# Kernel tuning notes

Measured on AMD Instinct MI355X. Metric: run time of the kernel, lower is better.

The kernel has to match this reference:

```python
import jax, jax.numpy as jnp
import numpy as np

DIM = 256
KEY_DIM = 16
NUM_HEADS = 8
ATTN_RATIO = 4
NH_KD = KEY_DIM * NUM_HEADS   # 128
D = ATTN_RATIO * KEY_DIM      # 64
DH = D * NUM_HEADS            # 512
POS_LEN = 16
SCALE = KEY_DIM ** -0.5


def _cbn(x, w, s, b):
    # 1x1 conv (no bias) + folded BatchNorm affine. w: [out,in], x: [B,in,H,W]
    y = jnp.einsum('oi,bihw->bohw', w, x)
    return y * s[None, :, None, None] + b[None, :, None, None]


def _interp_pos(pos, n):
    # F.interpolate(mode='linear', align_corners=False) from length POS_LEN to n.
    L = pos.shape[-1]
    coords = (jnp.arange(n, dtype=pos.dtype) + 0.5) * (L / n) - 0.5
    coords = jnp.clip(coords, 0.0, L - 1)
    lo = jnp.floor(coords).astype(jnp.int32)
    hi = jnp.minimum(lo + 1, L - 1)
    t = coords - lo.astype(pos.dtype)
    return pos[..., lo] * (1 - t) + pos[..., hi] * t  # [1,C,n]


def _axial_attn(q_emb, k_emb, v_emb, pos_q, pos_k, n):
    # q_emb/k_emb: [B,NH_KD,n], v_emb: [B,DH,n]
    B = q_emb.shape[0]
    q = (q_emb + _interp_pos(pos_q, n)).reshape(B, NUM_HEADS, KEY_DIM, n)
    k = (k_emb + _interp_pos(pos_k, n)).reshape(B, NUM_HEADS, KEY_DIM, n)
    v = v_emb.reshape(B, NUM_HEADS, D, n)
    attn = jnp.einsum('bhcn,bhcm->bhnm', q, k) * SCALE
    attn = jax.nn.softmax(attn, axis=-1)
    xx = jnp.einsum('bhnm,bhdm->bhnd', attn, v)      # [B,NH,n,D]
    return xx.transpose(0, 1, 3, 2).reshape(B, DH, n)  # [B,DH,n]


def _forward(x, wq, sq, bq, wk, sk, bk, wv, sv, bv,
             pos_rowq, pos_rowk, pos_colq, pos_colk,
             w_row, s_row, b_row, w_col, s_col, b_col,
             w_proj, s_proj, b_proj, w_sc, s_sc, b_sc,
             w_dw, s_dw, b_dw, w_pw, s_pw, b_pw):
    B, C, H, W = x.shape
    q = _cbn(x, wq, sq, bq)   # [B,NH_KD,H,W]
    k = _cbn(x, wk, sk, bk)
    v = _cbn(x, wv, sv, bv)   # [B,DH,H,W]

    # row branch (mean over W)
    xx_row = _axial_attn(q.mean(-1), k.mean(-1), v.mean(-1), pos_rowq, pos_rowk, H)
    xx_row = _cbn(jax.nn.relu(xx_row[..., None]), w_row, s_row, b_row)      # [B,DH,H,1]
    # column branch (mean over H)
    xx_col = _axial_attn(q.mean(-2), k.mean(-2), v.mean(-2), pos_colq, pos_colk, W)
    xx_col = _cbn(jax.nn.relu(xx_col[:, :, None, :]), w_col, s_col, b_col)  # [B,DH,1,W]

    attn_out = v + (xx_row + xx_col)
    attn_out = _cbn(jax.nn.relu(attn_out), w_proj, s_proj, b_proj)          # [B,DIM,H,W]

    # gate branch: 1x1 -> dw3x3 -> relu -> 1x1 -> h_sigmoid
    gate = _cbn(x, w_sc, s_sc, b_sc)
    gate = jax.lax.conv_general_dilated(
        gate, w_dw, (1, 1), 'SAME',
        dimension_numbers=('NCHW', 'OIHW', 'NCHW'), feature_group_count=DIM)
    gate = gate * s_dw[None, :, None, None] + b_dw[None, :, None, None]
    gate = jax.nn.relu(gate)
    gate = _cbn(gate, w_pw, s_pw, b_pw)
    gate = jnp.clip(gate + 3.0, 0.0, 6.0) / 6.0  # h_sigmoid
    return gate * attn_out


def setup_inputs() -> dict:
    key = jax.random.key(0)
    ks = jax.random.split(key, 32)
    B, H, W = 16, 64, 64
    nrm = lambda k, sh, sc=0.05: jax.random.normal(k, sh, dtype=jnp.float32) * sc
    inp = {
        'x': nrm(ks[0], (B, DIM, H, W), 1.0),
        'wq': nrm(ks[1], (NH_KD, DIM)), 'sq': 1.0 + nrm(ks[2], (NH_KD,)), 'bq': nrm(ks[3], (NH_KD,)),
        'wk': nrm(ks[4], (NH_KD, DIM)), 'sk': 1.0 + nrm(ks[5], (NH_KD,)), 'bk': nrm(ks[6], (NH_KD,)),
        'wv': nrm(ks[7], (DH, DIM)), 'sv': 1.0 + nrm(ks[8], (DH,)), 'bv': nrm(ks[9], (DH,)),
        'pos_rowq': nrm(ks[10], (1, NH_KD, POS_LEN), 1.0), 'pos_rowk': nrm(ks[11], (1, NH_KD, POS_LEN), 1.0),
        'pos_colq': nrm(ks[12], (1, NH_KD, POS_LEN), 1.0), 'pos_colk': nrm(ks[13], (1, NH_KD, POS_LEN), 1.0),
        'w_row': nrm(ks[14], (DH, DH)), 's_row': 1.0 + nrm(ks[15], (DH,)), 'b_row': nrm(ks[16], (DH,)),
        'w_col': nrm(ks[17], (DH, DH)), 's_col': 1.0 + nrm(ks[18], (DH,)), 'b_col': nrm(ks[19], (DH,)),
        'w_proj': nrm(ks[20], (DIM, DH)), 's_proj': 1.0 + nrm(ks[21], (DIM,)), 'b_proj': nrm(ks[22], (DIM,)),
        'w_sc': nrm(ks[23], (DIM, DIM)), 's_sc': 1.0 + nrm(ks[24], (DIM,)), 'b_sc': nrm(ks[25], (DIM,)),
        'w_dw': nrm(ks[26], (DIM, 1, 3, 3)), 's_dw': 1.0 + nrm(ks[27], (DIM,)), 'b_dw': nrm(ks[28], (DIM,)),
        'w_pw': nrm(ks[29], (DIM, DIM)), 's_pw': 1.0 + nrm(ks[30], (DIM,)), 'b_pw': nrm(ks[31], (DIM,)),
    }
    return inp


def reference(x, wq, sq, bq, wk, sk, bk, wv, sv, bv,
              pos_rowq, pos_rowk, pos_colq, pos_colk,
              w_row, s_row, b_row, w_col, s_col, b_col,
              w_proj, s_proj, b_proj, w_sc, s_sc, b_sc,
              w_dw, s_dw, b_dw, w_pw, s_pw, b_pw):
    return _forward(x, wq, sq, bq, wk, sk, bk, wv, sv, bv,
                    pos_rowq, pos_rowk, pos_colq, pos_colk,
                    w_row, s_row, b_row, w_col, s_col, b_col,
                    w_proj, s_proj, b_proj, w_sc, s_sc, b_sc,
                    w_dw, s_dw, b_dw, w_pw, s_pw, b_pw)
```

## Files before the change

### kernel.cpp

```cpp
#include <hip/hip_runtime.h>
#include <math.h>

typedef unsigned short u16;
typedef unsigned int u32;
typedef short short8 __attribute__((ext_vector_type(8)));
typedef float f32x4 __attribute__((ext_vector_type(4)));

#define Bn 16
#define Cc 256
#define Pp 4096
#define DHc 512
#define PTOT 65536
#define SCALE 0.25f

__device__ __forceinline__ float bf2f(u16 u) {
    return __uint_as_float(((u32)u) << 16);
}
__device__ __forceinline__ u16 f2bf(float f) {
    u32 u = __float_as_uint(f);
    u32 lsb = (u >> 16) & 1u;
    u += 0x7fffu + lsb;
    return (u16)(u >> 16);
}

__device__ __forceinline__ void gload16(const u16* g, u16* l) {
    __builtin_amdgcn_global_load_lds(
        (const __attribute__((address_space(1))) void*)(uintptr_t)g,
        (__attribute__((address_space(3))) void*)(u32)(uintptr_t)l,
        16, 0, 0);
}

__global__ __launch_bounds__(256) void mean_kernel(
    const float* __restrict__ x, u16* __restrict__ xmb) {
    __shared__ float plane[64][65];
    int bc = blockIdx.x;
    int b = bc >> 8, c = bc & 255;
    const float* xp = x + (size_t)bc * Pp;
    int tid = threadIdx.x;
#pragma unroll
    for (int k = 0; k < 16; ++k) {
        int idx = tid + k * 256;
        plane[idx >> 6][idx & 63] = xp[idx];
    }
    __syncthreads();
    if (tid < 64) {
        float s = 0.f;
#pragma unroll
        for (int w = 0; w < 64; ++w) s += plane[tid][w];
        xmb[((size_t)b * 64 + tid) * 256 + c] = f2bf(s * (1.f / 64.f));
    } else if (tid < 128) {
        int w = tid - 64;
        float s = 0.f;
#pragma unroll
        for (int h = 0; h < 64; ++h) s += plane[h][w];
        xmb[((size_t)1024 + b * 64 + w) * 256 + c] = f2bf(s * (1.f / 64.f));
    }
}

__global__ __launch_bounds__(256) void xpose_kernel(
    const float* __restrict__ x, u16* __restrict__ xbf) {
    __shared__ float tile[64][65];
    int pb = blockIdx.x;
    int cb = blockIdx.y;
    int b = blockIdx.z;
    int t = threadIdx.x;
    int p_l = t & 63, c_q = t >> 6;
    const float* xp = x + ((size_t)b * Cc + cb * 64) * Pp + pb * 64;
#pragma unroll
    for (int rr = 0; rr < 16; ++rr) {
        int c_l = rr * 4 + c_q;
        tile[p_l][c_l] = xp[(size_t)c_l * Pp + p_l];
    }
    __syncthreads();
    int c_l2 = t & 63, p_q = t >> 6;
    u16* dst = xbf + ((size_t)b * Pp + pb * 64) * Cc + cb * 64;
#pragma unroll
    for (int rr = 0; rr < 16; ++rr) {
        int p_l2 = rr * 4 + p_q;
        dst[(size_t)p_l2 * Cc + c_l2] = f2bf(tile[p_l2][c_l2]);
    }
}

__global__ __launch_bounds__(256) void wconv_kernel(
    const float* __restrict__ wq, const float* __restrict__ wk, const float* __restrict__ wv,
    const float* __restrict__ wsc, const float* __restrict__ wproj, const float* __restrict__ wpw,
    const float* __restrict__ wrow, const float* __restrict__ wcol,
    const float* __restrict__ wdw,
    u16* __restrict__ wqkvb, u16* __restrict__ wscb,
    u16* __restrict__ wprojb, u16* __restrict__ wpwb,
    u16* __restrict__ wrb, u16* __restrict__ wcb, float* __restrict__ wdwT) {
    int t = blockIdx.x * 256 + threadIdx.x;
    if (t < 2304) wdwT[(t % 9) * 256 + (t / 9)] = wdw[t];
    if (t < 32768) wqkvb[t] = f2bf(wq[t]);
    else if (t < 65536) wqkvb[t] = f2bf(wk[t - 32768]);
    else if (t < 196608) wqkvb[t] = f2bf(wv[t - 65536]);
    else if (t < 262144) wscb[t - 196608] = f2bf(wsc[t - 196608]);
    else if (t < 393216) wprojb[t - 262144] = f2bf(wproj[t - 262144]);
    else if (t < 458752) wpwb[t - 393216] = f2bf(wpw[t - 393216]);
    else if (t < 720896) wrb[t - 458752] = f2bf(wrow[t - 458752]);
    else wcb[t - 720896] = f2bf(wcol[t - 720896]);
}

__device__ __forceinline__ void gemm_mainloop(
    const u16* __restrict__ W, const u16* __restrict__ X, int K,
    int o0, size_t prow0, u16* ldsA, u16* ldsB, f32x4 (&acc)[4][4]) {
    int t = threadIdx.x;
    int w = t >> 6, lane = t & 63;
    int sr = (w << 5) + (lane >> 2);
    int ks = (lane & 3) * 8;
    const u16* gA = W + (size_t)(o0 + sr) * K + ks;
    const u16* gB = X + (prow0 + sr) * K + ks;
    u16* lA = ldsA + sr * 32 + ks;
    u16* lB = ldsB + sr * 32 + ks;
    int wo = (w >> 1) * 64, wp = (w & 1) * 64;
    const u16* fA = ldsA + (wo + (lane & 15)) * 32 + ((lane >> 4) * 8);
    const u16* fB = ldsB + (wp + (lane & 15)) * 32 + ((lane >> 4) * 8);

    for (int k0 = 0; k0 < K; k0 += 32) {
        if (k0) __syncthreads();
        gload16(gA + k0, lA);
        gload16(gA + k0 + (size_t)16 * K, lA + 16 * 32);
        gload16(gB + k0, lB);
        gload16(gB + k0 + (size_t)16 * K, lB + 16 * 32);
        __syncthreads();
        short8 a[4], b[4];
#pragma unroll
        for (int i = 0; i < 4; ++i) a[i] = *(const short8*)(fA + i * 16 * 32);
#pragma unroll
        for (int j = 0; j < 4; ++j) b[j] = *(const short8*)(fB + j * 16 * 32);
#pragma unroll
        for (int i = 0; i < 4; ++i)
#pragma unroll
            for (int j = 0; j < 4; ++j)
                acc[i][j] = __builtin_amdgcn_mfma_f32_16x16x32_bf16(a[i], b[j], acc[i][j], 0, 0, 0);
    }
}

__global__ __launch_bounds__(256) void gemm_qkv(
    const u16* __restrict__ Wb, const u16* __restrict__ X,
    const float* __restrict__ sq, const float* __restrict__ bq,
    const float* __restrict__ sk, const float* __restrict__ bk,
    const float* __restrict__ sv, const float* __restrict__ bv,
    const float* __restrict__ posrq, const float* __restrict__ posrk,
    const float* __restrict__ poscq, const float* __restrict__ posck,
    float* __restrict__ qrow, float* __restrict__ krow, float* __restrict__ vrow,
    float* __restrict__ qcol, float* __restrict__ kcol, float* __restrict__ vcol) {
    __shared__ u16 ldsA[128 * 32];
    __shared__ u16 ldsB[128 * 32];
    f32x4 acc[4][4];
#pragma unroll
    for (int i = 0; i < 4; ++i)
#pragma unroll
        for (int j = 0; j < 4; ++j) acc[i][j] = (f32x4){0.f, 0.f, 0.f, 0.f};
    int o0 = blockIdx.x * 128;
    size_t prow0 = (size_t)blockIdx.y * 128;
    gemm_mainloop(Wb, X, 256, o0, prow0, ldsA, ldsB, acc);

    int lane = threadIdx.x & 63, w = threadIdx.x >> 6;
    int wo = (w >> 1) * 64, wp = (w & 1) * 64;
    int quad = lane >> 4, cn = lane & 15;
#pragma unroll
    for (int j = 0; j < 4; ++j) {
        int p = (int)prow0 + wp + j * 16 + cn;
        int branch = p >> 10, loc = p & 1023;
        int b = loc >> 6, n = loc & 63;
        float coords = 0.25f * (float)n - 0.375f;
        coords = fminf(fmaxf(coords, 0.f), 15.f);
        int lo = (int)floorf(coords);
        int hi = min(lo + 1, 15);
        float tt = coords - (float)lo;
#pragma unroll
        for (int i = 0; i < 4; ++i) {
            int o = o0 + wo + i * 16 + quad * 4;
            if (o < 128) {
                const float* pos = branch ? poscq : posrq;
                float* dst = branch ? qcol : qrow;
#pragma unroll
                for (int r = 0; r < 4; ++r) {
                    int c = o + r;
                    float pv = pos[c * 16 + lo] * (1.f - tt) + pos[c * 16 + hi] * tt;
                    dst[b * 8192 + c * 64 + n] = acc[i][j][r] * sq[c] + bq[c] + pv;
                }
            } else if (o < 256) {
                const float* pos = branch ? posck : posrk;
                float* dst = branch ? kcol : krow;
#pragma unroll
                for (int r = 0; r < 4; ++r) {
                    int c = o - 128 + r;
                    float pv = pos[c * 16 + lo] * (1.f - tt) + pos[c * 16 + hi] * tt;
                    dst[b * 8192 + c * 64 + n] = acc[i][j][r] * sk[c] + bk[c] + pv;
                }
            } else {
                float* dst = branch ? vcol : vrow;
#pragma unroll
                for (int r = 0; r < 4; ++r) {
                    int c = o - 256 + r;
                    dst[b * 32768 + c * 64 + n] = acc[i][j][r] * sv[c] + bv[c];
                }
            }
        }
    }
}

__global__ __launch_bounds__(512, 2) void attn_kernel(
    const float* __restrict__ qr, const float* __restrict__ kr, const float* __restrict__ vr,
    const float* __restrict__ qc, const float* __restrict__ kc, const float* __restrict__ vc,
    u16* __restrict__ xxbf) {
    int branch = blockIdx.y;
    const float* q = branch ? qc : qr;
    const float* k = branch ? kc : kr;
    const float* v = branch ? vc : vr;
    int bh = blockIdx.x;
    int b = bh >> 3, h = bh & 7;
    __shared__ float qs[16][64], ks[16][64], vs[64][64];
    int t = threadIdx.x;
#pragma unroll
    for (int i = t; i < 1024; i += 512) {
        int c = i >> 6, nn = i & 63;
        qs[c][nn] = q[b * 8192 + (h * 16 + c) * 64 + nn];
        ks[c][nn] = k[b * 8192 + (h * 16 + c) * 64 + nn];
    }
#pragma unroll
    for (int i = t; i < 4096; i += 512) {
        int d = i >> 6, nn = i & 63;
        vs[d][nn] = v[b * 32768 + (h * 64 + d) * 64 + nn];
    }
    __syncthreads();

    int n = t & 63, dq = t >> 6;
    float qv[16];
#pragma unroll
    for (int c = 0; c < 16; ++c) qv[c] = qs[c][n];

    float s_[64];
    float mx = -1e30f;
#pragma unroll
    for (int m = 0; m < 64; ++m) {
        float acc = 0.f;
#pragma unroll
        for (int c = 0; c < 16; ++c) acc += qv[c] * ks[c][m];
        acc *= SCALE;
        s_[m] = acc;
        mx = fmaxf(mx, acc);
    }
    float sum = 0.f;
#pragma unroll
    for (int m = 0; m < 64; ++m) {
        s_[m] = __expf(s_[m] - mx);
        sum += s_[m];
    }
    float inv = 1.f / sum;
    u16* dst = xxbf + (((size_t)(b * 2 + branch)) * 64 + n) * 512 + h * 64 + dq * 8;
#pragma unroll
    for (int dd = 0; dd < 8; ++dd) {
        int d = dq * 8 + dd;
        float acc = 0.f;
#pragma unroll
        for (int m = 0; m < 64; ++m) acc += s_[m] * vs[d][m];
        dst[dd] = f2bf(fmaxf(acc * inv, 0.f));
    }
}

__global__ __launch_bounds__(256) void post_gemm(
    const u16* __restrict__ xxbf, const u16* __restrict__ wrb, const u16* __restrict__ wcb,
    const float* __restrict__ s_row, const float* __restrict__ b_row,
    const float* __restrict__ s_col, const float* __restrict__ b_col,
    float* __restrict__ xr2, float* __restrict__ xc2) {
    __shared__ u16 ldsA[64 * 32];
    __shared__ u16 ldsB[256 * 32];
    int o0 = blockIdx.x * 256;
    int b = blockIdx.y;
    int branch = blockIdx.z;
    const u16* A = xxbf + ((size_t)(b * 2 + branch)) * 64 * 512;
    const u16* W = branch ? wcb : wrb;
    const float* ss = branch ? s_col : s_row;
    const float* bb = branch ? b_col : b_row;
    float* dst = (branch ? xc2 : xr2) + (size_t)b * 32768;

    f32x4 acc[4][4];
#pragma unroll
    for (int i = 0; i < 4; ++i)
#pragma unroll
        for (int j = 0; j < 4; ++j) acc[i][j] = (f32x4){0.f, 0.f, 0.f, 0.f};

    int t = threadIdx.x, w = t >> 6, lane = t & 63;
    int ks = (t & 3) * 8;
    const u16* gA = A + (size_t)(t >> 2) * 512 + ks;
    const u16* gB = W + (size_t)(o0 + (t >> 2)) * 512 + ks;
    u16* lA = ldsA + (t >> 2) * 32 + ks;
    u16* lB = ldsB + (t >> 2) * 32 + ks;
    const u16* fA = ldsA + (lane & 15) * 32 + ((lane >> 4) * 8);
    const u16* fB = ldsB + (w * 64 + (lane & 15)) * 32 + ((lane >> 4) * 8);

    for (int k0 = 0; k0 < 512; k0 += 32) {
        if (k0) __syncthreads();
        gload16(gA + k0, lA);
#pragma unroll
        for (int r = 0; r < 4; ++r)
            gload16(gB + k0 + (size_t)r * 64 * 512, lB + r * 64 * 32);
        __syncthreads();
        short8 a[4], bfr[4];
#pragma unroll
        for (int i = 0; i < 4; ++i) a[i] = *(const short8*)(fA + i * 16 * 32);
#pragma unroll
        for (int j = 0; j < 4; ++j) bfr[j] = *(const short8*)(fB + j * 16 * 32);
#pragma unroll
        for (int i = 0; i < 4; ++i)
#pragma unroll
            for (int j = 0; j < 4; ++j)
                acc[i][j] = __builtin_amdgcn_mfma_f32_16x16x32_bf16(a[i], bfr[j], acc[i][j], 0, 0, 0);
    }

    int quad = lane >> 4, cn = lane & 15;
#pragma unroll
    for (int i = 0; i < 4; ++i)
#pragma unroll
        for (int j = 0; j < 4; ++j) {
            int o = o0 + w * 64 + j * 16 + cn;
            float sv_ = ss[o], bv_ = bb[o];
#pragma unroll
            for (int r = 0; r < 4; ++r) {
                int n = i * 16 + quad * 4 + r;
                dst[n * 512 + o] = acc[i][j][r] * sv_ + bv_;
            }
        }
}

__global__ __launch_bounds__(512, 4) void gemm_cbn64(
    const u16* __restrict__ Wb, const u16* __restrict__ X,
    const float* __restrict__ s, const float* __restrict__ bb,
    u16* __restrict__ outb, int hsig) {
    __shared__ u16 lds[64 * 256];

    int t = threadIdx.x;
    int lane = t & 63, w = t >> 6;
    int quad = lane >> 4, cn = lane & 15;
    int p0 = blockIdx.x * 64;

#pragma unroll
    for (int r = 0; r < 4; ++r) {
        int li = r * 512 + t;
        int p = li >> 5, ko = li & 31;
        gload16(X + ((size_t)(p0 + p)) * 256 + ((ko ^ (p & 7)) << 3),
                lds + (size_t)li * 8);
    }
    __syncthreads();

    f32x4 acc[2][4];
#pragma unroll
    for (int i = 0; i < 2; ++i)
#pragma unroll
        for (int j = 0; j < 4; ++j) acc[i][j] = (f32x4){0.f, 0.f, 0.f, 0.f};

    int ow = w * 32;
    const u16* gA = Wb + (size_t)(ow + cn) * 256 + quad * 8;

    short8 a_c[2], b_c[4];
#pragma unroll
    for (int i = 0; i < 2; ++i) a_c[i] = *(const short8*)(gA + (size_t)i * 16 * 256);
    {
        int og0 = quad;
#pragma unroll
        for (int j = 0; j < 4; ++j) {
            int pl = j * 16 + cn;
            b_c[j] = *(const short8*)&lds[pl * 256 + ((og0 ^ (pl & 7)) << 3)];
        }
    }

#pragma unroll
    for (int kk = 0; kk < 8; ++kk) {
        short8 a_n[2], b_n[4];
        if (kk < 7) {
            int k1 = kk * 32 + 32;
#pragma unroll
            for (int i = 0; i < 2; ++i)
                a_n[i] = *(const short8*)(gA + (size_t)i * 16 * 256 + k1);
            int og = (k1 >> 3) + quad;
#pragma unroll
            for (int j = 0; j < 4; ++j) {
                int pl = j * 16 + cn;
                b_n[j] = *(const short8*)&lds[pl * 256 + ((og ^ (pl & 7)) << 3)];
            }
        }
#pragma unroll
        for (int i = 0; i < 2; ++i)
#pragma unroll
            for (int j = 0; j < 4; ++j)
                acc[i][j] = __builtin_amdgcn_mfma_f32_16x16x32_bf16(a_c[i], b_c[j], acc[i][j], 0, 0, 0);
        if (kk < 7) {
#pragma unroll
            for (int i = 0; i < 2; ++i) a_c[i] = a_n[i];
#pragma unroll
            for (int j = 0; j < 4; ++j) b_c[j] = b_n[j];
        }
    }

#pragma unroll
    for (int i = 0; i < 2; ++i) {
        int ob = ow + i * 16 + quad * 4;
        f32x4 s4 = *(const f32x4*)&s[ob];
        f32x4 b4 = *(const f32x4*)&bb[ob];
#pragma unroll
        for (int j = 0; j < 4; ++j) {
            size_t p = (size_t)p0 + j * 16 + cn;
            ushort4 o4;
            if (hsig) {
                o4.x = f2bf(fminf(fmaxf(acc[i][j][0] * s4[0] + b4[0] + 3.f, 0.f), 6.f) * (1.f / 6.f));
                o4.y = f2bf(fminf(fmaxf(acc[i][j][1] * s4[1] + b4[1] + 3.f, 0.f), 6.f) * (1.f / 6.f));
                o4.z = f2bf(fminf(fmaxf(acc[i][j][2] * s4[2] + b4[2] + 3.f, 0.f), 6.f) * (1.f / 6.f));
                o4.w = f2bf(fminf(fmaxf(acc[i][j][3] * s4[3] + b4[3] + 3.f, 0.f), 6.f) * (1.f / 6.f));
            } else {
                o4.x = f2bf(acc[i][j][0] * s4[0] + b4[0]);
                o4.y = f2bf(acc[i][j][1] * s4[1] + b4[1]);
                o4.z = f2bf(acc[i][j][2] * s4[2] + b4[2]);
                o4.w = f2bf(acc[i][j][3] * s4[3] + b4[3]);
            }
            *(ushort4*)&outb[p * 256 + ob] = o4;
        }
    }
}

__global__ __launch_bounds__(512, 4) void fused_vproj(
    const u16* __restrict__ Wv, const u16* __restrict__ Wp,
    const u16* __restrict__ X,
    const float* __restrict__ sv, const float* __restrict__ bv,
    const float* __restrict__ xr2, const float* __restrict__ xc2,
    const float* __restrict__ sp, const float* __restrict__ bp,
    const u16* __restrict__ gate, float* __restrict__ out) {
    __shared__ u16 lds[64 * 512];

    int t = threadIdx.x;
    int lane = t & 63, w = t >> 6;
    int quad = lane >> 4, cn = lane & 15;
    int p0 = blockIdx.x * 64;
    int bi = p0 >> 12;
    int hh = (p0 >> 6) & 63;

#pragma unroll
    for (int r = 0; r < 4; ++r) {
        int li = r * 512 + t;
        int p = li >> 5, ko = li & 31;
        gload16(X + ((size_t)(p0 + p)) * 256 + ((ko ^ (p & 7)) << 3),
                lds + (size_t)li * 8);
    }
    __syncthreads();

    f32x4 acc1[4][4];
#pragma unroll
    for (int i = 0; i < 4; ++i)
#pragma unroll
        for (int j = 0; j < 4; ++j) acc1[i][j] = (f32x4){0.f, 0.f, 0.f, 0.f};

    int ow = w * 64;
    const u16* gA = Wv + (size_t)(ow + cn) * 256 + quad * 8;

    short8 a_c[4];
#pragma unroll
    for (int i = 0; i < 4; ++i) a_c[i] = *(const short8*)(gA + (size_t)i * 16 * 256);

#pragma unroll
    for (int kk = 0; kk < 8; ++kk) {
        int k0 = kk * 32;
        short8 a_n[4];
        if (kk < 7) {
#pragma unroll
            for (int i = 0; i < 4; ++i)
                a_n[i] = *(const short8*)(gA + (size_t)i * 16 * 256 + k0 + 32);
        }
        int og = (k0 >> 3) + quad;
        short8 b[4];
#pragma unroll
        for (int j = 0; j < 4; ++j) {
            int pl = j * 16 + cn;
            b[j] = *(const short8*)&lds[pl * 256 + ((og ^ (pl & 7)) << 3)];
        }
#pragma unroll
        for (int i = 0; i < 4; ++i)
#pragma unroll
            for (int j = 0; j < 4; ++j)
                acc1[i][j] = __builtin_amdgcn_mfma_f32_16x16x32_bf16(a_c[i], b[j], acc1[i][j], 0, 0, 0);
        if (kk < 7) {
#pragma unroll
            for (int i = 0; i < 4; ++i) a_c[i] = a_n[i];
        }
    }

    __syncthreads();

#pragma unroll
    for (int i = 0; i < 4; ++i) {
        int ob = ow + i * 16 + quad * 4;
        f32x4 s4 = *(const f32x4*)&sv[ob];
        f32x4 b4 = *(const f32x4*)&bv[ob];
        f32x4 ra = *(const f32x4*)&xr2[(size_t)bi * 32768 + hh * 512 + ob];
#pragma unroll
        for (int j = 0; j < 4; ++j) {
            int p = j * 16 + cn;
            f32x4 ca = *(const f32x4*)&xc2[(size_t)bi * 32768 + p * 512 + ob];
            ushort4 o4;
            o4.x = f2bf(fmaxf(acc1[i][j][0] * s4[0] + b4[0] + ra[0] + ca[0], 0.f));
            o4.y = f2bf(fmaxf(acc1[i][j][1] * s4[1] + b4[1] + ra[1] + ca[1], 0.f));
            o4.z = f2bf(fmaxf(acc1[i][j][2] * s4[2] + b4[2] + ra[2] + ca[2], 0.f));
            o4.w = f2bf(fmaxf(acc1[i][j][3] * s4[3] + b4[3] + ra[3] + ca[3], 0.f));
            *(ushort4*)&lds[p * 512 + (ob ^ ((p & 7) << 3))] = o4;
        }
    }
    __syncthreads();

    f32x4 acc2[2][4];
#pragma unroll
    for (int i = 0; i < 2; ++i)
#pragma unroll
        for (int j = 0; j < 4; ++j) acc2[i][j] = (f32x4){0.f, 0.f, 0.f, 0.f};

    int o2w = w * 32;
    const u16* gP = Wp + (size_t)(o2w + cn) * 512 + quad * 8;

    short8 a2_c[2], b2_c[4];
#pragma unroll
    for (int i = 0; i < 2; ++i) a2_c[i] = *(const short8*)(gP + (size_t)i * 16 * 512);
    {
        int kk0 = quad * 8;
#pragma unroll
        for (int j = 0; j < 4; ++j) {
            int p = j * 16 + cn;
            b2_c[j] = *(const short8*)&lds[p * 512 + (kk0 ^ ((p & 7) << 3))];
        }
    }

#pragma unroll
    for (int kk = 0; kk < 16; ++kk) {
        short8 a2_n[2], b2_n[4];
        if (kk < 15) {
            int k1 = kk * 32 + 32;
#pragma unroll
            for (int i = 0; i < 2; ++i)
                a2_n[i] = *(const short8*)(gP + (size_t)i * 16 * 512 + k1);
            int kn = k1 + quad * 8;
#pragma unroll
            for (int j = 0; j < 4; ++j) {
                int p = j * 16 + cn;
                b2_n[j] = *(const short8*)&lds[p * 512 + (kn ^ ((p & 7) << 3))];
            }
        }
#pragma unroll
        for (int i = 0; i < 2; ++i)
#pragma unroll
            for (int j = 0; j < 4; ++j)
                acc2[i][j] = __builtin_amdgcn_mfma_f32_16x16x32_bf16(a2_c[i], b2_c[j], acc2[i][j], 0, 0, 0);
        if (kk < 15) {
#pragma unroll
            for (int i = 0; i < 2; ++i) a2_c[i] = a2_n[i];
#pragma unroll
            for (int j = 0; j < 4; ++j) b2_c[j] = b2_n[j];
        }
    }

    int pl0 = p0 & 4095;
#pragma unroll
    for (int i = 0; i < 2; ++i) {
        int ob = o2w + i * 16 + quad * 4;
        f32x4 s4 = *(const f32x4*)&sp[ob];
        f32x4 b4 = *(const f32x4*)&bp[ob];
#pragma unroll
        for (int j = 0; j < 4; ++j) {
            int p = j * 16 + cn;
            size_t pg = (size_t)p0 + p;
            ushort4 gv = *(const ushort4*)&gate[pg * 256 + ob];
            float* op = out + (size_t)bi * 1048576 + (size_t)ob * 4096 + (pl0 + p);
            op[0 * 4096] = bf2f(gv.x) * (acc2[i][j][0] * s4[0] + b4[0]);
            op[1 * 4096] = bf2f(gv.y) * (acc2[i][j][1] * s4[1] + b4[1]);
            op[2 * 4096] = bf2f(gv.z) * (acc2[i][j][2] * s4[2] + b4[2]);
            op[3 * 4096] = bf2f(gv.w) * (acc2[i][j][3] * s4[3] + b4[3]);
        }
    }
}

__global__ __launch_bounds__(256) void dw_kernel(
    const u16* __restrict__ sc, const float* __restrict__ wdwT,
    const float* __restrict__ sdw, const float* __restrict__ bdw, u16* __restrict__ dwout) {
    int t = blockIdx.x * 256 + threadIdx.x;
    int cg = (t & 31) * 8;
    size_t p = (size_t)(t >> 5);
    int h = (int)((p >> 6) & 63), w_ = (int)(p & 63);
    float acc[8] = {0.f, 0.f, 0.f, 0.f, 0.f, 0.f, 0.f, 0.f};
#pragma unroll
    for (int ky = 0; ky < 3; ++ky) {
        int hh = h + ky - 1;
        if (hh < 0 || hh > 63) continue;
#pragma unroll
        for (int kx = 0; kx < 3; ++kx) {
            int wx = w_ + kx - 1;
            if (wx < 0 || wx > 63) continue;
            size_t pp = (size_t)((long long)p + (ky - 1) * 64 + (kx - 1));
            short8 v = *(const short8*)&sc[pp * 256 + cg];
            const float* wt = &wdwT[(ky * 3 + kx) * 256 + cg];
            f32x4 w0 = *(const f32x4*)wt;
            f32x4 w1 = *(const f32x4*)(wt + 4);
            acc[0] += w0[0] * bf2f((u16)v[0]); acc[1] += w0[1] * bf2f((u16)v[1]);
            acc[2] += w0[2] * bf2f((u16)v[2]); acc[3] += w0[3] * bf2f((u16)v[3]);
            acc[4] += w1[0] * bf2f((u16)v[4]); acc[5] += w1[1] * bf2f((u16)v[5]);
            acc[6] += w1[2] * bf2f((u16)v[6]); acc[7] += w1[3] * bf2f((u16)v[7]);
        }
    }
    f32x4 s0 = *(const f32x4*)&sdw[cg], s1 = *(const f32x4*)&sdw[cg + 4];
    f32x4 b0 = *(const f32x4*)&bdw[cg], b1 = *(const f32x4*)&bdw[cg + 4];
    short8 o;
    o[0] = (short)f2bf(fmaxf(acc[0] * s0[0] + b0[0], 0.f));
    o[1] = (short)f2bf(fmaxf(acc[1] * s0[1] + b0[1], 0.f));
    o[2] = (short)f2bf(fmaxf(acc[2] * s0[2] + b0[2], 0.f));
    o[3] = (short)f2bf(fmaxf(acc[3] * s0[3] + b0[3], 0.f));
    o[4] = (short)f2bf(fmaxf(acc[4] * s1[0] + b1[0], 0.f));
    o[5] = (short)f2bf(fmaxf(acc[5] * s1[1] + b1[1], 0.f));
    o[6] = (short)f2bf(fmaxf(acc[6] * s1[2] + b1[2], 0.f));
    o[7] = (short)f2bf(fmaxf(acc[7] * s1[3] + b1[3], 0.f));
    *(short8*)&dwout[p * 256 + cg] = o;
}

extern "C" void kernel_launch(void* const* d_in, const int* in_sizes, int n_in,
                              void* d_out, int out_size, void* d_ws, size_t ws_size,
                              hipStream_t stream) {
    const float* x = (const float*)d_in[0];
    const float* wq = (const float*)d_in[1];
    const float* sq = (const float*)d_in[2];
    const float* bq = (const float*)d_in[3];
    const float* wk = (const float*)d_in[4];
    const float* sk = (const float*)d_in[5];
    const float* bk = (const float*)d_in[6];
    const float* wv = (const float*)d_in[7];
    const float* sv = (const float*)d_in[8];
    const float* bv = (const float*)d_in[9];
    const float* posrq = (const float*)d_in[10];
    const float* posrk = (const float*)d_in[11];
    const float* poscq = (const float*)d_in[12];
    const float* posck = (const float*)d_in[13];
    const float* w_row = (const float*)d_in[14];
    const float* s_row = (const float*)d_in[15];
    const float* b_row = (const float*)d_in[16];
    const float* w_col = (const float*)d_in[17];
    const float* s_col = (const float*)d_in[18];
    const float* b_col = (const float*)d_in[19];
    const float* w_proj = (const float*)d_in[20];
    const float* s_proj = (const float*)d_in[21];
    const float* b_proj = (const float*)d_in[22];
    const float* w_sc = (const float*)d_in[23];
    const float* s_sc = (const float*)d_in[24];
    const float* b_sc = (const float*)d_in[25];
    const float* w_dw = (const float*)d_in[26];
    const float* s_dw = (const float*)d_in[27];
    const float* b_dw = (const float*)d_in[28];
    const float* w_pw = (const float*)d_in[29];
    const float* s_pw = (const float*)d_in[30];
    const float* b_pw = (const float*)d_in[31];
    float* out = (float*)d_out;

    float* fws = (float*)d_ws;
    float* qrow = fws;
    float* krow = qrow + 131072;
    float* qcol = krow + 131072;
    float* kcol = qcol + 131072;
    float* vrow = kcol + 131072;
    float* vcol = vrow + 524288;
    float* xr2  = vcol + 524288;
    float* xc2  = xr2 + 524288;
    float* wdwT = xc2 + 524288;
    u16* xmb    = (u16*)(wdwT + 2304);
    u16* xbf    = xmb + 524288;
    u16* wqkvb  = xbf + (size_t)PTOT * 256;
    u16* wscb   = wqkvb + 196608;
    u16* wprojb = wscb + 65536;
    u16* wpwb   = wprojb + 131072;
    u16* wrb    = wpwb + 65536;
    u16* wcb    = wrb + 262144;
    u16* xxbf   = wcb + 262144;
    u16* scb    = xxbf + 1048576;
    u16* dwb    = scb + (size_t)PTOT * 256;
    u16* gate   = scb;

    mean_kernel<<<dim3(Bn * Cc), 256, 0, stream>>>(x, xmb);
    xpose_kernel<<<dim3(64, 4, Bn), 256, 0, stream>>>(x, xbf);
    wconv_kernel<<<dim3(3840), 256, 0, stream>>>(
        wq, wk, wv, w_sc, w_proj, w_pw, w_row, w_col, w_dw,
        wqkvb, wscb, wprojb, wpwb, wrb, wcb, wdwT);
    gemm_qkv<<<dim3(6, 16), 256, 0, stream>>>(
        wqkvb, xmb, sq, bq, sk, bk, sv, bv,
        posrq, posrk, poscq, posck, qrow, krow, vrow, qcol, kcol, vcol);
    attn_kernel<<<dim3(128, 2), 512, 0, stream>>>(qrow, krow, vrow, qcol, kcol, vcol, xxbf);
    post_gemm<<<dim3(2, Bn, 2), 256, 0, stream>>>(
        xxbf, wrb, wcb, s_row, b_row, s_col, b_col, xr2, xc2);
    gemm_cbn64<<<dim3(1024), 512, 0, stream>>>(wscb, xbf, s_sc, b_sc, scb, 0);
    dw_kernel<<<dim3(8192), 256, 0, stream>>>(scb, wdwT, s_dw, b_dw, dwb);
    gemm_cbn64<<<dim3(1024), 512, 0, stream>>>(wpwb, dwb, s_pw, b_pw, gate, 1);
    fused_vproj<<<dim3(1024), 512, 0, stream>>>(
        wqkvb + 65536, wprojb, xbf, sv, bv, xr2, xc2, s_proj, b_proj, gate, out);
}
```

Before: 420.4 us.

## Fuse depthwise conv into pointwise GEMM and retile shortcut GEMM

```diff
diff --git a/kernel.cpp b/kernel.cpp
--- a/kernel.cpp
+++ b/kernel.cpp
@@ -326,96 +326,137 @@
         }
 }
 
-__global__ __launch_bounds__(512, 4) void gemm_cbn64(
+__global__ __launch_bounds__(256) void gemm_sc(
     const u16* __restrict__ Wb, const u16* __restrict__ X,
-    const float* __restrict__ s, const float* __restrict__ bb,
-    u16* __restrict__ outb, int hsig) {
-    __shared__ u16 lds[64 * 256];
+    const float* __restrict__ s, const float* __restrict__ bb, u16* __restrict__ outb) {
+    __shared__ u16 ldsA[128 * 32];
+    __shared__ u16 ldsB[128 * 32];
+    f32x4 acc[4][4];
+#pragma unroll
+    for (int i = 0; i < 4; ++i)
+#pragma unroll
+        for (int j = 0; j < 4; ++j) acc[i][j] = (f32x4){0.f, 0.f, 0.f, 0.f};
+    int o0 = blockIdx.x * 128;
+    size_t prow0 = (size_t)blockIdx.y * 128;
+    gemm_mainloop(Wb, X, 256, o0, prow0, ldsA, ldsB, acc);
+
+    int lane = threadIdx.x & 63, w = threadIdx.x >> 6;
+    int wo = (w >> 1) * 64, wp = (w & 1) * 64;
+    int quad = lane >> 4, cn = lane & 15;
+#pragma unroll
+    for (int i = 0; i < 4; ++i) {
+        int ob = o0 + wo + i * 16 + quad * 4;
+        f32x4 s4 = *(const f32x4*)&s[ob];
+        f32x4 b4 = *(const f32x4*)&bb[ob];
+#pragma unroll
+        for (int j = 0; j < 4; ++j) {
+            size_t p = prow0 + wp + j * 16 + cn;
+            ushort4 o4;
+            o4.x = f2bf(acc[i][j][0] * s4[0] + b4[0]);
+            o4.y = f2bf(acc[i][j][1] * s4[1] + b4[1]);
+            o4.z = f2bf(acc[i][j][2] * s4[2] + b4[2]);
+            o4.w = f2bf(acc[i][j][3] * s4[3] + b4[3]);
+            *(ushort4*)&outb[p * 256 + ob] = o4;
+        }
+    }
+}
+
+__global__ __launch_bounds__(512, 4) void fused_dwpw(
+    const u16* __restrict__ sc, const float* __restrict__ wdwT,
+    const float* __restrict__ sdw, const float* __restrict__ bdw,
+    const u16* __restrict__ Wpw,
+    const float* __restrict__ spw, const float* __restrict__ bpw,
+    u16* __restrict__ gate) {
+    __shared__ u16 dwt[64 * 256];
 
     int t = threadIdx.x;
     int lane = t & 63, w = t >> 6;
     int quad = lane >> 4, cn = lane & 15;
     int p0 = blockIdx.x * 64;
-
-#pragma unroll
-    for (int r = 0; r < 4; ++r) {
-        int li = r * 512 + t;
-        int p = li >> 5, ko = li & 31;
-        gload16(X + ((size_t)(p0 + p)) * 256 + ((ko ^ (p & 7)) << 3),
-                lds + (size_t)li * 8);
+    int h = (p0 >> 6) & 63;
+
+#pragma unroll
+    for (int kq = 0; kq < 4; ++kq) {
+        int task = t + kq * 512;
+        int p_l = task >> 5;
+        int cg = (task & 31) * 8;
+        size_t p = (size_t)p0 + p_l;
+        float acc[8] = {0.f, 0.f, 0.f, 0.f, 0.f, 0.f, 0.f, 0.f};
+#pragma unroll
+        for (int ky = 0; ky < 3; ++ky) {
+            int hh = h + ky - 1;
+            if (hh < 0 || hh > 63) continue;
+#pragma unroll
+            for (int kx = 0; kx < 3; ++kx) {
+                int wx = p_l + kx - 1;
+                if (wx < 0 || wx > 63) continue;
+                size_t pp = (size_t)((long long)p + (ky - 1) * 64 + (kx - 1));
+                short8 v = *(const short8*)&sc[pp * 256 + cg];
+                const float* wt = &wdwT[(ky * 3 + kx) * 256 + cg];
+                f32x4 w0 = *(const f32x4*)wt;
+                f32x4 w1 = *(const f32x4*)(wt + 4);
+                acc[0] += w0[0] * bf2f((u16)v[0]); acc[1] += w0[1] * bf2f((u16)v[1]);
+                acc[2] += w0[2] * bf2f((u16)v[2]); acc[3] += w0[3] * bf2f((u16)v[3]);
+                acc[4] += w1[0] * bf2f((u16)v[4]); acc[5] += w1[1] * bf2f((u16)v[5]);
+                acc[6] += w1[2] * bf2f((u16)v[6]); acc[7] += w1[3] * bf2f((u16)v[7]);
+            }
+        }
+        f32x4 s0 = *(const f32x4*)&sdw[cg], s1 = *(const f32x4*)&sdw[cg + 4];
+        f32x4 b0 = *(const f32x4*)&bdw[cg], b1 = *(const f32x4*)&bdw[cg + 4];
+        short8 o;
+        o[0] = (short)f2bf(fmaxf(acc[0] * s0[0] + b0[0], 0.f));
+        o[1] = (short)f2bf(fmaxf(acc[1] * s0[1] + b0[1], 0.f));
+        o[2] = (short)f2bf(fmaxf(acc[2] * s0[2] + b0[2], 0.f));
+        o[3] = (short)f2bf(fmaxf(acc[3] * s0[3] + b0[3], 0.f));
+        o[4] = (short)f2bf(fmaxf(acc[4] * s1[0] + b1[0], 0.f));
+        o[5] = (short)f2bf(fmaxf(acc[5] * s1[1] + b1[1], 0.f));
+        o[6] = (short)f2bf(fmaxf(acc[6] * s1[2] + b1[2], 0.f));
+        o[7] = (short)f2bf(fmaxf(acc[7] * s1[3] + b1[3], 0.f));
+        int ko = cg >> 3;
+        *(short8*)&dwt[p_l * 256 + ((ko ^ (p_l & 7)) << 3)] = o;
     }
     __syncthreads();
 
-    f32x4 acc[2][4];
+    f32x4 acc2[2][4];
 #pragma unroll
     for (int i = 0; i < 2; ++i)
 #pragma unroll
-        for (int j = 0; j < 4; ++j) acc[i][j] = (f32x4){0.f, 0.f, 0.f, 0.f};
+        for (int j = 0; j < 4; ++j) acc2[i][j] = (f32x4){0.f, 0.f, 0.f, 0.f};
 
     int ow = w * 32;
-    const u16* gA = Wb + (size_t)(ow + cn) * 256 + quad * 8;
-
-    short8 a_c[2], b_c[4];
-#pragma unroll
-    for (int i = 0; i < 2; ++i) a_c[i] = *(const short8*)(gA + (size_t)i * 16 * 256);
-    {
-        int og0 = quad;
+    const u16* gA = Wpw + (size_t)(ow + cn) * 256 + quad * 8;
+
+    for (int k0 = 0; k0 < 256; k0 += 32) {
+        short8 a[2], b[4];
+        a[0] = *(const short8*)(gA + k0);
+        a[1] = *(const short8*)(gA + (size_t)16 * 256 + k0);
+        int og = (k0 >> 3) + quad;
 #pragma unroll
         for (int j = 0; j < 4; ++j) {
             int pl = j * 16 + cn;
-            b_c[j] = *(const short8*)&lds[pl * 256 + ((og0 ^ (pl & 7)) << 3)];
-        }
-    }
-
-#pragma unroll
-    for (int kk = 0; kk < 8; ++kk) {
-        short8 a_n[2], b_n[4];
-        if (kk < 7) {
-            int k1 = kk * 32 + 32;
-#pragma unroll
-            for (int i = 0; i < 2; ++i)
-                a_n[i] = *(const short8*)(gA + (size_t)i * 16 * 256 + k1);
-            int og = (k1 >> 3) + quad;
-#pragma unroll
-            for (int j = 0; j < 4; ++j) {
-                int pl = j * 16 + cn;
-                b_n[j] = *(const short8*)&lds[pl * 256 + ((og ^ (pl & 7)) << 3)];
-            }
+            b[j] = *(const short8*)&dwt[pl * 256 + ((og ^ (pl & 7)) << 3)];
         }
 #pragma unroll
         for (int i = 0; i < 2; ++i)
 #pragma unroll
             for (int j = 0; j < 4; ++j)
-                acc[i][j] = __builtin_amdgcn_mfma_f32_16x16x32_bf16(a_c[i], b_c[j], acc[i][j], 0, 0, 0);
-        if (kk < 7) {
-#pragma unroll
-            for (int i = 0; i < 2; ++i) a_c[i] = a_n[i];
-#pragma unroll
-            for (int j = 0; j < 4; ++j) b_c[j] = b_n[j];
-        }
+                acc2[i][j] = __builtin_amdgcn_mfma_f32_16x16x32_bf16(a[i], b[j], acc2[i][j], 0, 0, 0);
     }
 
 #pragma unroll
     for (int i = 0; i < 2; ++i) {
         int ob = ow + i * 16 + quad * 4;
-        f32x4 s4 = *(const f32x4*)&s[ob];
-        f32x4 b4 = *(const f32x4*)&bb[ob];
+        f32x4 s4 = *(const f32x4*)&spw[ob];
+        f32x4 b4 = *(const f32x4*)&bpw[ob];
 #pragma unroll
         for (int j = 0; j < 4; ++j) {
             size_t p = (size_t)p0 + j * 16 + cn;
             ushort4 o4;
-            if (hsig) {
-                o4.x = f2bf(fminf(fmaxf(acc[i][j][0] * s4[0] + b4[0] + 3.f, 0.f), 6.f) * (1.f / 6.f));
-                o4.y = f2bf(fminf(fmaxf(acc[i][j][1] * s4[1] + b4[1] + 3.f, 0.f), 6.f) * (1.f / 6.f));
-                o4.z = f2bf(fminf(fmaxf(acc[i][j][2] * s4[2] + b4[2] + 3.f, 0.f), 6.f) * (1.f / 6.f));
-                o4.w = f2bf(fminf(fmaxf(acc[i][j][3] * s4[3] + b4[3] + 3.f, 0.f), 6.f) * (1.f / 6.f));
-            } else {
-                o4.x = f2bf(acc[i][j][0] * s4[0] + b4[0]);
-                o4.y = f2bf(acc[i][j][1] * s4[1] + b4[1]);
-                o4.z = f2bf(acc[i][j][2] * s4[2] + b4[2]);
-                o4.w = f2bf(acc[i][j][3] * s4[3] + b4[3]);
-            }
-            *(ushort4*)&outb[p * 256 + ob] = o4;
+            o4.x = f2bf(fminf(fmaxf(acc2[i][j][0] * s4[0] + b4[0] + 3.f, 0.f), 6.f) * (1.f / 6.f));
+            o4.y = f2bf(fminf(fmaxf(acc2[i][j][1] * s4[1] + b4[1] + 3.f, 0.f), 6.f) * (1.f / 6.f));
+            o4.z = f2bf(fminf(fmaxf(acc2[i][j][2] * s4[2] + b4[2] + 3.f, 0.f), 6.f) * (1.f / 6.f));
+            o4.w = f2bf(fminf(fmaxf(acc2[i][j][3] * s4[3] + b4[3] + 3.f, 0.f), 6.f) * (1.f / 6.f));
+            *(ushort4*)&gate[p * 256 + ob] = o4;
         }
     }
 }
@@ -574,47 +615,6 @@
             op[3 * 4096] = bf2f(gv.w) * (acc2[i][j][3] * s4[3] + b4[3]);
         }
     }
-}
-
-__global__ __launch_bounds__(256) void dw_kernel(
-    const u16* __restrict__ sc, const float* __restrict__ wdwT,
-    const float* __restrict__ sdw, const float* __restrict__ bdw, u16* __restrict__ dwout) {
-    int t = blockIdx.x * 256 + threadIdx.x;
-    int cg = (t & 31) * 8;
-    size_t p = (size_t)(t >> 5);
-    int h = (int)((p >> 6) & 63), w_ = (int)(p & 63);
-    float acc[8] = {0.f, 0.f, 0.f, 0.f, 0.f, 0.f, 0.f, 0.f};
-#pragma unroll
-    for (int ky = 0; ky < 3; ++ky) {
-        int hh = h + ky - 1;
-        if (hh < 0 || hh > 63) continue;
-#pragma unroll
-        for (int kx = 0; kx < 3; ++kx) {
-            int wx = w_ + kx - 1;
-            if (wx < 0 || wx > 63) continue;
-            size_t pp = (size_t)((long long)p + (ky - 1) * 64 + (kx - 1));
-            short8 v = *(const short8*)&sc[pp * 256 + cg];
-            const float* wt = &wdwT[(ky * 3 + kx) * 256 + cg];
-            f32x4 w0 = *(const f32x4*)wt;
-            f32x4 w1 = *(const f32x4*)(wt + 4);
-            acc[0] += w0[0] * bf2f((u16)v[0]); acc[1] += w0[1] * bf2f((u16)v[1]);
-            acc[2] += w0[2] * bf2f((u16)v[2]); acc[3] += w0[3] * bf2f((u16)v[3]);
-            acc[4] += w1[0] * bf2f((u16)v[4]); acc[5] += w1[1] * bf2f((u16)v[5]);
-            acc[6] += w1[2] * bf2f((u16)v[6]); acc[7] += w1[3] * bf2f((u16)v[7]);
-        }
-    }
-    f32x4 s0 = *(const f32x4*)&sdw[cg], s1 = *(const f32x4*)&sdw[cg + 4];
-    f32x4 b0 = *(const f32x4*)&bdw[cg], b1 = *(const f32x4*)&bdw[cg + 4];
-    short8 o;
-    o[0] = (short)f2bf(fmaxf(acc[0] * s0[0] + b0[0], 0.f));
-    o[1] = (short)f2bf(fmaxf(acc[1] * s0[1] + b0[1], 0.f));
-    o[2] = (short)f2bf(fmaxf(acc[2] * s0[2] + b0[2], 0.f));
-    o[3] = (short)f2bf(fmaxf(acc[3] * s0[3] + b0[3], 0.f));
-    o[4] = (short)f2bf(fmaxf(acc[4] * s1[0] + b1[0], 0.f));
-    o[5] = (short)f2bf(fmaxf(acc[5] * s1[1] + b1[1], 0.f));
-    o[6] = (short)f2bf(fmaxf(acc[6] * s1[2] + b1[2], 0.f));
-    o[7] = (short)f2bf(fmaxf(acc[7] * s1[3] + b1[3], 0.f));
-    *(short8*)&dwout[p * 256 + cg] = o;
 }
 
 extern "C" void kernel_launch(void* const* d_in, const int* in_sizes, int n_in,
@@ -674,8 +674,7 @@
     u16* wcb    = wrb + 262144;
     u16* xxbf   = wcb + 262144;
     u16* scb    = xxbf + 1048576;
-    u16* dwb    = scb + (size_t)PTOT * 256;
-    u16* gate   = scb;
+    u16* gate   = scb + (size_t)PTOT * 256;
 
     mean_kernel<<<dim3(Bn * Cc), 256, 0, stream>>>(x, xmb);
     xpose_kernel<<<dim3(64, 4, Bn), 256, 0, stream>>>(x, xbf);
@@ -688,9 +687,9 @@
     attn_kernel<<<dim3(128, 2), 512, 0, stream>>>(qrow, krow, vrow, qcol, kcol, vcol, xxbf);
     post_gemm<<<dim3(2, Bn, 2), 256, 0, stream>>>(
         xxbf, wrb, wcb, s_row, b_row, s_col, b_col, xr2, xc2);
-    gemm_cbn64<<<dim3(1024), 512, 0, stream>>>(wscb, xbf, s_sc, b_sc, scb, 0);
-    dw_kernel<<<dim3(8192), 256, 0, stream>>>(scb, wdwT, s_dw, b_dw, dwb);
-    gemm_cbn64<<<dim3(1024), 512, 0, stream>>>(wpwb, dwb, s_pw, b_pw, gate, 1);
+    gemm_sc<<<dim3(2, 512), 256, 0, stream>>>(wscb, xbf, s_sc, b_sc, scb);
+    fused_dwpw<<<dim3(1024), 512, 0, stream>>>(
+        scb, wdwT, s_dw, b_dw, wpwb, s_pw, b_pw, gate);
     fused_vproj<<<dim3(1024), 512, 0, stream>>>(
         wqkvb + 65536, wprojb, xbf, sv, bv, xr2, xc2, s_proj, b_proj, gate, out);
 }
```

New measurement: 405.5 us. 1.04x faster.
